# Optimization experiments

Measured on AMD Instinct MI355X. Metric: run time of the kernel, lower is better.

The kernel has to match this reference:

```python
import jax, jax.numpy as jnp
import numpy as np

B, IN_DIM, K, D = 8192, 1024, 2048, 256
TAU = 1.0
BN_EPS = 1e-5


def setup_inputs() -> dict:
    key = jax.random.key(0)
    ks = jax.random.split(key, 4)
    x = jax.random.normal(ks[0], (B, IN_DIM), dtype=jnp.float32)
    u = jax.random.uniform(ks[1], (B, K), dtype=jnp.float32)  # uniform for gumbel noise
    W = jax.random.normal(ks[2], (IN_DIM, D), dtype=jnp.float32) * 0.02
    b = jnp.zeros((D,), dtype=jnp.float32)
    gamma = jnp.ones((D,), dtype=jnp.float32)
    beta = jnp.zeros((D,), dtype=jnp.float32)
    E = jax.random.normal(ks[3], (K, D), dtype=jnp.float32)  # nn.Embedding default N(0,1)
    return {"x": x, "u": u, "W": W, "b": b, "gamma": gamma, "beta": beta, "E": E}


def reference(x, u, W, b, gamma, beta, E):
    # classifier + BatchNorm1d (training mode: batch stats, biased variance)
    h = x @ W + b                                   # [B, D]
    mu = jnp.mean(h, axis=0)
    var = jnp.var(h, axis=0)
    h = (h - mu) * jax.lax.rsqrt(var + BN_EPS) * gamma + beta
    # negative squared euclidean distance via ||h||^2 - 2 h.E^T + ||e||^2 (GEMM form,
    # avoids materializing [B, K, D])
    h2 = jnp.sum(h * h, axis=-1, keepdims=True)     # [B, 1]
    e2 = jnp.sum(E * E, axis=-1)                    # [K]
    logits = -(h2 - 2.0 * (h @ E.T) + e2)           # [B, K]
    # gumbel-softmax (soft) with tau
    g = -jnp.log(-jnp.log(u + 1e-10) + 1e-10)
    assignments = jax.nn.softmax((logits + g) / TAU, axis=-1)  # [B, K]
    z = assignments @ E                             # [B, D]
    probs = jax.nn.softmax(logits, axis=-1)
    return probs, z
```

## Files before the change

kernel.cpp:

```cpp
#include <hip/hip_runtime.h>
#include <math.h>

#define B_SZ 8192
#define IN_DIM 1024
#define K_CB 2048
#define D_SZ 256
#define BN_EPS 1e-5f

typedef _Float16 f16;
typedef _Float16 f16x8 __attribute__((ext_vector_type(8)));
typedef _Float16 f16x4 __attribute__((ext_vector_type(4)));
typedef float    f32x4 __attribute__((ext_vector_type(4)));

#define GLOAD_LDS16(g, l) __builtin_amdgcn_global_load_lds(                      \
    (const __attribute__((address_space(1))) unsigned int*)(g),                  \
    (__attribute__((address_space(3))) unsigned int*)(l), 16, 0, 0)

template<int BM, int BN, int BK, int EPI, bool A32>
__global__ __launch_bounds__(256) void gemm_mfma(
    const void* __restrict__ Aptr, int lda,
    const f16* __restrict__ Bptr, int ldb,
    void* __restrict__ Cptr, int ldc, int Kdim,
    const float* __restrict__ bias)
{
    constexpr int G    = BK / 8;
    constexpr int MASK = G - 1;
    constexpr int WM = BM / 2, WN = BN / 2;
    constexpr int FM = WM / 16, FN = WN / 16;
    constexpr int CH_A = BM * G;
    constexpr int CH_B = BN * G;

    __shared__ char lds[(BM + BN) * BK * 2];
    char* As = lds;
    char* Bs = lds + BM * BK * 2;

    const int tid  = threadIdx.x;
    const int w    = tid >> 6, lane = tid & 63;
    const int wm   = w >> 1,   wn   = w & 1;
    const int row0 = blockIdx.x * BM;
    const int col0 = blockIdx.y * BN;

    f32x4 acc[FM][FN] = {};

    for (int k0 = 0; k0 < Kdim; k0 += BK) {
        #pragma unroll
        for (int i = 0; i < CH_B / 256; ++i) {
            const int base = (i * 4 + w) * 64;
            const int s = base + lane;
            const int r = s / G, c = s % G;
            const f16* src = Bptr + (size_t)(col0 + r) * ldb + k0 + ((c ^ (r & MASK)) * 8);
            GLOAD_LDS16(src, Bs + base * 16);
        }
        if (!A32) {
            #pragma unroll
            for (int i = 0; i < CH_A / 256; ++i) {
                const int base = (i * 4 + w) * 64;
                const int s = base + lane;
                const int r = s / G, c = s % G;
                const f16* src = (const f16*)Aptr + (size_t)(row0 + r) * lda + k0 + ((c ^ (r & MASK)) * 8);
                GLOAD_LDS16(src, As + base * 16);
            }
        } else {
            #pragma unroll
            for (int i = 0; i < CH_A / 256; ++i) {
                const int s = i * 256 + tid;
                const int r = s / G, c = s % G;
                const float* src = (const float*)Aptr + (size_t)(row0 + r) * lda + k0 + c * 8;
                const float4 v0 = ((const float4*)src)[0];
                const float4 v1 = ((const float4*)src)[1];
                f16x8 d;
                d[0] = (f16)v0.x; d[1] = (f16)v0.y; d[2] = (f16)v0.z; d[3] = (f16)v0.w;
                d[4] = (f16)v1.x; d[5] = (f16)v1.y; d[6] = (f16)v1.z; d[7] = (f16)v1.w;
                *(f16x8*)(As + (r * G + (c ^ (r & MASK))) * 16) = d;
            }
        }
        __syncthreads();

        #pragma unroll
        for (int kk = 0; kk < BK / 32; ++kk) {
            f16x8 af[FM], bf[FN];
            #pragma unroll
            for (int m = 0; m < FM; ++m) {
                const int r = wm * WM + m * 16 + (lane & 15);
                const int g = (kk * 4 + (lane >> 4)) ^ (r & MASK);
                af[m] = *(const f16x8*)(As + r * (BK * 2) + g * 16);
            }
            #pragma unroll
            for (int n = 0; n < FN; ++n) {
                const int r = wn * WN + n * 16 + (lane & 15);
                const int g = (kk * 4 + (lane >> 4)) ^ (r & MASK);
                bf[n] = *(const f16x8*)(Bs + r * (BK * 2) + g * 16);
            }
            #pragma unroll
            for (int m = 0; m < FM; ++m)
                #pragma unroll
                for (int n = 0; n < FN; ++n)
                    acc[m][n] = __builtin_amdgcn_mfma_f32_16x16x32_f16(af[m], bf[n], acc[m][n], 0, 0, 0);
        }
        __syncthreads();
    }

    #pragma unroll
    for (int m = 0; m < FM; ++m) {
        const int rbase = row0 + wm * WM + m * 16 + (lane >> 4) * 4;
        #pragma unroll
        for (int n = 0; n < FN; ++n) {
            const int c = col0 + wn * WN + n * 16 + (lane & 15);
            #pragma unroll
            for (int j = 0; j < 4; ++j) {
                const float v = acc[m][n][j];
                if (EPI == 0) {
                    ((float*)Cptr)[(size_t)(rbase + j) * ldc + c] = v;
                } else {
                    ((f16*)Cptr)[(size_t)(rbase + j) * ldc + c] = (f16)(v + bias[c]);
                }
            }
        }
    }
}

#define LP1 2056

__global__ __launch_bounds__(1024, 1) void fused_sm(
    const f16* __restrict__ h16, const f16* __restrict__ E16,
    const float* __restrict__ e2v, const float* __restrict__ u,
    const float* __restrict__ scale, const float* __restrict__ shift,
    float* __restrict__ probs, f16* __restrict__ assign16)
{
    __shared__ __align__(16) char lds_raw[32 * LP1 * 2];
    __shared__ float redA[16 * 16];
    f16* Bs0 = (f16*)lds_raw;
    f16* Bs1 = Bs0 + 128 * 256;
    f16* p1buf = (f16*)lds_raw;

    const int tid  = threadIdx.x;
    const int w    = tid >> 6, lane = tid & 63;
    const int q    = lane >> 4, r16 = lane & 15;
    const int g2   = w >> 3;
    const int wc   = w & 7;
    const int row0 = blockIdx.x * 32;
    const int rowA = row0 + g2 * 16;
    const int colL = wc * 16 + r16;

    f16x8 af[8];
    {
        const f16* hrow = h16 + (size_t)(rowA + r16) * D_SZ + q * 8;
        #pragma unroll
        for (int kk = 0; kk < 8; ++kk) {
            const f16x8 raw = *(const f16x8*)(hrow + kk * 32);
            const float4 scA = *(const float4*)(scale + kk * 32 + q * 8);
            const float4 scB = *(const float4*)(scale + kk * 32 + q * 8 + 4);
            const float4 shA = *(const float4*)(shift + kk * 32 + q * 8);
            const float4 shB = *(const float4*)(shift + kk * 32 + q * 8 + 4);
            f16x8 d;
            d[0] = (f16)fmaf((float)raw[0], scA.x, shA.x);
            d[1] = (f16)fmaf((float)raw[1], scA.y, shA.y);
            d[2] = (f16)fmaf((float)raw[2], scA.z, shA.z);
            d[3] = (f16)fmaf((float)raw[3], scA.w, shA.w);
            d[4] = (f16)fmaf((float)raw[4], scB.x, shB.x);
            d[5] = (f16)fmaf((float)raw[5], scB.y, shB.y);
            d[6] = (f16)fmaf((float)raw[6], scB.z, shB.z);
            d[7] = (f16)fmaf((float)raw[7], scB.w, shB.w);
            af[kk] = d;
        }
    }

    f32x4 acc[16];
    #pragma unroll
    for (int n = 0; n < 16; ++n) acc[n] = (f32x4){0.f, 0.f, 0.f, 0.f};

    #pragma unroll
    for (int i = 0; i < 4; ++i) {
        const int base = (i * 16 + w) * 64;
        const int s = base + lane;
        const int r = s >> 5, cgg = s & 31;
        GLOAD_LDS16(E16 + (size_t)r * D_SZ + ((cgg ^ (r & 31)) * 8), Bs0 + base * 8);
    }

    #pragma unroll
    for (int c = 0; c < 16; ++c) {
        f16* buf  = (c & 1) ? Bs1 : Bs0;
        f16* nbuf = (c & 1) ? Bs0 : Bs1;
        if (c < 15) {
            #pragma unroll
            for (int i = 0; i < 4; ++i) {
                const int base = (i * 16 + w) * 64;
                const int s = base + lane;
                const int r = s >> 5, cgg = s & 31;
                GLOAD_LDS16(E16 + (size_t)((c + 1) * 128 + r) * D_SZ + ((cgg ^ (r & 31)) * 8),
                            nbuf + base * 8);
            }
            asm volatile("s_waitcnt vmcnt(4)" ::: "memory");
        } else {
            asm volatile("s_waitcnt vmcnt(0)" ::: "memory");
        }
        __builtin_amdgcn_s_barrier();
        __builtin_amdgcn_sched_barrier(0);
        #pragma unroll
        for (int kk = 0; kk < 8; ++kk) {
            const int gb = (kk * 4 + q) ^ (colL & 31);
            const f16x8 bf = *(const f16x8*)(buf + colL * 256 + gb * 8);
            acc[c] = __builtin_amdgcn_mfma_f32_16x16x32_f16(af[kk], bf, acc[c], 0, 0, 0);
        }
        __builtin_amdgcn_sched_barrier(0);
        __builtin_amdgcn_s_barrier();
        __builtin_amdgcn_sched_barrier(0);
    }
    __syncthreads();

    float m1[4] = {-1e30f, -1e30f, -1e30f, -1e30f};
    #pragma unroll
    for (int n = 0; n < 16; ++n) {
        const float ec = e2v[n * 128 + colL];
        #pragma unroll
        for (int j = 0; j < 4; ++j)
            m1[j] = fmaxf(m1[j], 2.f * acc[n][j] - ec);
    }
    #pragma unroll
    for (int off = 1; off < 16; off <<= 1)
        #pragma unroll
        for (int j = 0; j < 4; ++j)
            m1[j] = fmaxf(m1[j], __shfl_xor(m1[j], off));
    if (r16 == 0)
        #pragma unroll
        for (int j = 0; j < 4; ++j) redA[w * 16 + q * 4 + j] = m1[j];
    __syncthreads();
    #pragma unroll
    for (int j = 0; j < 4; ++j) {
        float a = -1e30f;
        #pragma unroll
        for (int t = 0; t < 8; ++t) a = fmaxf(a, redA[(g2 * 8 + t) * 16 + q * 4 + j]);
        m1[j] = a;
    }

    #pragma unroll
    for (int n = 0; n < 16; ++n) {
        const float ec = e2v[n * 128 + colL];
        #pragma unroll
        for (int j = 0; j < 4; ++j) {
            const float lv = 2.f * acc[n][j] - ec;
            p1buf[(size_t)(g2 * 16 + q * 4 + j) * LP1 + n * 128 + colL] =
                (f16)__expf(lv - m1[j] + 10.f);
        }
    }
    __syncthreads();

    const int trow = tid >> 5;
    const int cg   = tid & 31;
    const float* urow = u + (size_t)(row0 + trow) * K_CB + cg * 4;
    const f16* prow_l = p1buf + (size_t)trow * LP1 + cg * 4;

    float s1 = 0.f, s2 = 0.f;
    f16x4 gv[16];
    #pragma unroll
    for (int n = 0; n < 16; ++n) {
        const float4 u4 = *(const float4*)(urow + n * 128);
        const f16x4 p4 = *(const f16x4*)(prow_l + n * 128);
        const float ua[4] = {u4.x, u4.y, u4.z, u4.w};
        #pragma unroll
        for (int e = 0; e < 4; ++e) {
            const f16 g = (f16)(-__logf(-__logf(ua[e] + 1e-10f) + 1e-10f));
            gv[n][e] = g;
            s1 += (float)p4[e];
            s2 += (float)p4[e] * __expf((float)g);
        }
    }
    #pragma unroll
    for (int off = 1; off < 32; off <<= 1) {
        s1 += __shfl_xor(s1, off);
        s2 += __shfl_xor(s2, off);
    }
    const float r1 = 1.f / s1;
    const float r2 = 1.f / s2;

    float* prow = probs + (size_t)(row0 + trow) * K_CB + cg * 4;
    f16* arow = assign16 + (size_t)(row0 + trow) * K_CB + cg * 4;
    #pragma unroll
    for (int n = 0; n < 16; ++n) {
        const f16x4 p4 = *(const f16x4*)(prow_l + n * 128);
        float4 o;
        o.x = (float)p4[0] * r1; o.y = (float)p4[1] * r1;
        o.z = (float)p4[2] * r1; o.w = (float)p4[3] * r1;
        *(float4*)(prow + n * 128) = o;
        f16x4 a4;
        #pragma unroll
        for (int e = 0; e < 4; ++e)
            a4[e] = (f16)((float)p4[e] * __expf((float)gv[n][e]) * r2);
        *(f16x4*)(arow + n * 128) = a4;
    }
}

__global__ __launch_bounds__(256) void conv_WT(const float* __restrict__ W, f16* __restrict__ WT)
{
    const int r = blockIdx.x, c = threadIdx.x;
    WT[c * 1024 + r] = (f16)W[r * 256 + c];
}

__global__ __launch_bounds__(256) void conv_E2(const float* __restrict__ E,
                                               f16* __restrict__ E16, f16* __restrict__ ET,
                                               float* __restrict__ e2)
{
    const int r = blockIdx.x, c = threadIdx.x;
    const int wave = c >> 6, lane = c & 63;
    const float v = E[r * 256 + c];
    E16[r * 256 + c] = (f16)v;
    ET[c * 2048 + r] = (f16)v;
    float ss = v * v;
    #pragma unroll
    for (int off = 32; off > 0; off >>= 1) ss += __shfl_down(ss, off);
    __shared__ float s4[4];
    if (lane == 0) s4[wave] = ss;
    __syncthreads();
    if (c == 0) e2[r] = s4[0] + s4[1] + s4[2] + s4[3];
}

__global__ __launch_bounds__(256) void bn_partial(const f16* __restrict__ h16, float* __restrict__ part)
{
    const int d = threadIdx.x;
    const int blk = blockIdx.x;
    const int r0 = blk * (B_SZ / 128);
    float s = 0.f, sq = 0.f;
    for (int r = r0; r < r0 + (B_SZ / 128); ++r) {
        const float v = (float)h16[(size_t)r * D_SZ + d];
        s += v; sq += v * v;
    }
    part[blk * 512 + d]       = s;
    part[blk * 512 + 256 + d] = sq;
}

__global__ __launch_bounds__(256) void bn_finalize(
    const float* __restrict__ part, const float* __restrict__ gamma, const float* __restrict__ beta,
    float* __restrict__ scale, float* __restrict__ shift)
{
    const int d = threadIdx.x;
    float s = 0.f, sq = 0.f;
    for (int b = 0; b < 128; ++b) { s += part[b * 512 + d]; sq += part[b * 512 + 256 + d]; }
    const float mu  = s / (float)B_SZ;
    const float var = sq / (float)B_SZ - mu * mu;
    const float sc  = gamma[d] * rsqrtf(var + BN_EPS);
    scale[d] = sc;
    shift[d] = beta[d] - mu * sc;
}

extern "C" void kernel_launch(void* const* d_in, const int* in_sizes, int n_in,
                              void* d_out, int out_size, void* d_ws, size_t ws_size,
                              hipStream_t stream)
{
    const float* x     = (const float*)d_in[0];
    const float* u     = (const float*)d_in[1];
    const float* W     = (const float*)d_in[2];
    const float* bias  = (const float*)d_in[3];
    const float* gamma = (const float*)d_in[4];
    const float* beta  = (const float*)d_in[5];
    const float* E     = (const float*)d_in[6];

    float* probs = (float*)d_out;
    float* z     = probs + (size_t)B_SZ * K_CB;

    char* ws = (char*)d_ws;
    f16* assign16 = (f16*)ws;  ws += (size_t)B_SZ * K_CB * 2;
    f16* h16 = (f16*)ws;       ws += (size_t)B_SZ * D_SZ * 2;
    f16* WT16 = (f16*)ws;      ws += (size_t)D_SZ * IN_DIM * 2;
    f16* E16 = (f16*)ws;       ws += (size_t)K_CB * D_SZ * 2;
    f16* ET16 = (f16*)ws;      ws += (size_t)D_SZ * K_CB * 2;
    float* part = (float*)ws;  ws += 128 * 512 * 4;
    float* scale = (float*)ws; ws += D_SZ * 4;
    float* shift = (float*)ws; ws += D_SZ * 4;
    float* e2 = (float*)ws;    ws += K_CB * 4;

    conv_WT<<<IN_DIM, 256, 0, stream>>>(W, WT16);
    conv_E2<<<K_CB, 256, 0, stream>>>(E, E16, ET16, e2);

    {
        dim3 g(B_SZ / 64, D_SZ / 64);
        gemm_mfma<64, 64, 64, 1, true><<<g, 256, 0, stream>>>(
            x, IN_DIM, WT16, IN_DIM, h16, D_SZ, IN_DIM, bias);
    }
    bn_partial<<<128, 256, 0, stream>>>(h16, part);
    bn_finalize<<<1, 256, 0, stream>>>(part, gamma, beta, scale, shift);

    fused_sm<<<B_SZ / 32, 1024, 0, stream>>>(h16, E16, e2, u, scale, shift, probs, assign16);

    {
        dim3 g(B_SZ / 64, D_SZ / 64);
        gemm_mfma<64, 64, 128, 0, false><<<g, 256, 0, stream>>>(
            assign16, K_CB, ET16, K_CB, z, D_SZ, K_CB, nullptr);
    }
}
```

Before: 117.2 us.

## Move BN normalization to separate kernel and stage A tile in LDS

Batch-norm scale/shift now runs in a new standalone kernel that rewrites h16 in place, rather than inside fused_sm. fused_sm copies its 32-row A tile into a padded LDS buffer and reads A fragments from LDS on every MFMA step, instead of keeping them in registers. The aim is to free the per-wave A-fragment registers in the register-bound 1024-thread kernel. In exchange it adds an extra kernel launch, another pass over h16 in global memory, and extra LDS reads in the inner loop.

```diff
diff --git a/kernel.cpp b/kernel.cpp
--- a/kernel.cpp
+++ b/kernel.cpp
@@ -120,18 +120,19 @@
 }
 
 #define LP1 2056
+#define ATP 264
 
 __global__ __launch_bounds__(1024, 1) void fused_sm(
     const f16* __restrict__ h16, const f16* __restrict__ E16,
     const float* __restrict__ e2v, const float* __restrict__ u,
-    const float* __restrict__ scale, const float* __restrict__ shift,
     float* __restrict__ probs, f16* __restrict__ assign16)
 {
-    __shared__ __align__(16) char lds_raw[32 * LP1 * 2];
-    __shared__ float redA[16 * 16];
+    __shared__ __align__(16) char lds_raw[32 * LP1 * 2 + 32 * ATP * 2 + 16 * 16 * 4];
     f16* Bs0 = (f16*)lds_raw;
     f16* Bs1 = Bs0 + 128 * 256;
     f16* p1buf = (f16*)lds_raw;
+    f16* Atile = (f16*)(lds_raw + 32 * LP1 * 2);
+    float* redA = (float*)(lds_raw + 32 * LP1 * 2 + 32 * ATP * 2);
 
     const int tid  = threadIdx.x;
     const int w    = tid >> 6, lane = tid & 63;
@@ -139,30 +140,13 @@
     const int g2   = w >> 3;
     const int wc   = w & 7;
     const int row0 = blockIdx.x * 32;
-    const int rowA = row0 + g2 * 16;
     const int colL = wc * 16 + r16;
 
-    f16x8 af[8];
     {
-        const f16* hrow = h16 + (size_t)(rowA + r16) * D_SZ + q * 8;
-        #pragma unroll
-        for (int kk = 0; kk < 8; ++kk) {
-            const f16x8 raw = *(const f16x8*)(hrow + kk * 32);
-            const float4 scA = *(const float4*)(scale + kk * 32 + q * 8);
-            const float4 scB = *(const float4*)(scale + kk * 32 + q * 8 + 4);
-            const float4 shA = *(const float4*)(shift + kk * 32 + q * 8);
-            const float4 shB = *(const float4*)(shift + kk * 32 + q * 8 + 4);
-            f16x8 d;
-            d[0] = (f16)fmaf((float)raw[0], scA.x, shA.x);
-            d[1] = (f16)fmaf((float)raw[1], scA.y, shA.y);
-            d[2] = (f16)fmaf((float)raw[2], scA.z, shA.z);
-            d[3] = (f16)fmaf((float)raw[3], scA.w, shA.w);
-            d[4] = (f16)fmaf((float)raw[4], scB.x, shB.x);
-            d[5] = (f16)fmaf((float)raw[5], scB.y, shB.y);
-            d[6] = (f16)fmaf((float)raw[6], scB.z, shB.z);
-            d[7] = (f16)fmaf((float)raw[7], scB.w, shB.w);
-            af[kk] = d;
-        }
+        const int ar = tid >> 5;
+        const int ac = (tid & 31) * 8;
+        const f16x8 v = *(const f16x8*)(h16 + (size_t)(row0 + ar) * D_SZ + ac);
+        *(f16x8*)(Atile + ar * ATP + ac) = v;
     }
 
     f32x4 acc[16];
@@ -176,6 +160,9 @@
         const int r = s >> 5, cgg = s & 31;
         GLOAD_LDS16(E16 + (size_t)r * D_SZ + ((cgg ^ (r & 31)) * 8), Bs0 + base * 8);
     }
+    __syncthreads();
+
+    const f16* arow = Atile + (g2 * 16 + r16) * ATP + q * 8;
 
     #pragma unroll
     for (int c = 0; c < 16; ++c) {
@@ -198,9 +185,10 @@
         __builtin_amdgcn_sched_barrier(0);
         #pragma unroll
         for (int kk = 0; kk < 8; ++kk) {
+            const f16x8 a8 = *(const f16x8*)(arow + kk * 32);
             const int gb = (kk * 4 + q) ^ (colL & 31);
             const f16x8 bf = *(const f16x8*)(buf + colL * 256 + gb * 8);
-            acc[c] = __builtin_amdgcn_mfma_f32_16x16x32_f16(af[kk], bf, acc[c], 0, 0, 0);
+            acc[c] = __builtin_amdgcn_mfma_f32_16x16x32_f16(a8, bf, acc[c], 0, 0, 0);
         }
         __builtin_amdgcn_sched_barrier(0);
         __builtin_amdgcn_s_barrier();
@@ -274,7 +262,7 @@
     const float r2 = 1.f / s2;
 
     float* prow = probs + (size_t)(row0 + trow) * K_CB + cg * 4;
-    f16* arow = assign16 + (size_t)(row0 + trow) * K_CB + cg * 4;
+    f16* aout = assign16 + (size_t)(row0 + trow) * K_CB + cg * 4;
     #pragma unroll
     for (int n = 0; n < 16; ++n) {
         const f16x4 p4 = *(const f16x4*)(prow_l + n * 128);
@@ -286,7 +274,7 @@
         #pragma unroll
         for (int e = 0; e < 4; ++e)
             a4[e] = (f16)((float)p4[e] * __expf((float)gv[n][e]) * r2);
-        *(f16x4*)(arow + n * 128) = a4;
+        *(f16x4*)(aout + n * 128) = a4;
     }
 }
 
@@ -340,6 +328,22 @@
     const float sc  = gamma[d] * rsqrtf(var + BN_EPS);
     scale[d] = sc;
     shift[d] = beta[d] - mu * sc;
+}
+
+__global__ __launch_bounds__(256) void norm_h(
+    f16* __restrict__ h16, const float* __restrict__ scale, const float* __restrict__ shift)
+{
+    const int wave = threadIdx.x >> 6, lane = threadIdx.x & 63;
+    const int row = blockIdx.x * 4 + wave;
+    f16x4* hp = (f16x4*)(h16 + (size_t)row * D_SZ);
+    f16x4 v = hp[lane];
+    const float4 sc = ((const float4*)scale)[lane];
+    const float4 sh = ((const float4*)shift)[lane];
+    v[0] = (f16)fmaf((float)v[0], sc.x, sh.x);
+    v[1] = (f16)fmaf((float)v[1], sc.y, sh.y);
+    v[2] = (f16)fmaf((float)v[2], sc.z, sh.z);
+    v[3] = (f16)fmaf((float)v[3], sc.w, sh.w);
+    hp[lane] = v;
 }
 
 extern "C" void kernel_launch(void* const* d_in, const int* in_sizes, int n_in,
@@ -378,8 +382,9 @@
     }
     bn_partial<<<128, 256, 0, stream>>>(h16, part);
     bn_finalize<<<1, 256, 0, stream>>>(part, gamma, beta, scale, shift);
-
-    fused_sm<<<B_SZ / 32, 1024, 0, stream>>>(h16, E16, e2, u, scale, shift, probs, assign16);
+    norm_h<<<B_SZ / 4, 256, 0, stream>>>(h16, scale, shift);
+
+    fused_sm<<<B_SZ / 32, 1024, 0, stream>>>(h16, E16, e2, u, probs, assign16);
 
     {
         dim3 g(B_SZ / 64, D_SZ / 64);
```

After: 124.7 us. 1.06x slower.
